# Optimization experiments

Measured on AMD Instinct MI355X. Metric: run time of the kernel, lower is better.

Reference implementation:

```python
import jax, jax.numpy as jnp
import numpy as np

T, D = 1024, 1024            # tokens, model dim
E, K = 16, 4                 # routed experts, top-k
G, TG = 4, 2                 # expert groups, limited (top) groups
INTER = 512                  # moe_inter_dim
SHARED_INTER = 2 * INTER     # n_shared_experts * moe_inter_dim
ROUTE_SCALE = 2.5
STD = 0.02


def setup_inputs() -> dict:
    key = jax.random.key(0)
    ks = jax.random.split(key, 9)
    return {
        "x": jax.random.normal(ks[0], (T, D), jnp.float32),
        "token_mask": jnp.ones((T,), jnp.bool_),
        "gate_w": jax.random.normal(ks[1], (E, D), jnp.float32) * STD,
        "gate_bias": jnp.zeros((E,), jnp.float32),  # e_score_correction_bias (zero-init)
        "gate_projs": jax.random.normal(ks[2], (E, INTER, D), jnp.float32) * STD,
        "up_projs": jax.random.normal(ks[3], (E, INTER, D), jnp.float32) * STD,
        "down_projs": jax.random.normal(ks[4], (E, D, INTER), jnp.float32) * STD,
        "shared_gate": jax.random.normal(ks[5], (SHARED_INTER, D), jnp.float32) * STD,
        "shared_up": jax.random.normal(ks[6], (SHARED_INTER, D), jnp.float32) * STD,
        "shared_down": jax.random.normal(ks[7], (D, SHARED_INTER), jnp.float32) * STD,
    }


def _route(x, gate_w, gate_bias):
    # sigmoid scoring with e_score_correction_bias + group-limited top-k (DeepSeek-V3 style)
    scores = jax.nn.sigmoid(x @ gate_w.T)                      # [T, E]
    s = (scores + gate_bias).reshape(T, G, E // G)             # bias-corrected, grouped
    group_scores = jax.lax.top_k(s, 2)[0].sum(-1)              # [T, G] sum of top-2 per group
    gidx = jax.lax.top_k(group_scores, TG)[1]                  # [T, TG]
    gmask = jax.nn.one_hot(gidx, G, dtype=s.dtype).sum(1)      # [T, G] selected-group mask
    masked = (s * gmask[:, :, None]).reshape(T, E)
    idx = jax.lax.top_k(masked, K)[1]                          # [T, K] expert indices
    w = jnp.take_along_axis(scores, idx, axis=1)               # gather original (unbiased) scores
    w = w / w.sum(-1, keepdims=True) * ROUTE_SCALE             # sigmoid renorm + route scale
    return w.astype(x.dtype), idx


def reference(x, token_mask, gate_w, gate_bias, gate_projs, up_projs,
              down_projs, shared_gate, shared_up, shared_down):
    w, idx = _route(x, gate_w, gate_bias)
    # dense combine weights [T, E]: combine[t, e] = sum_k w[t, k] * (idx[t, k] == e)
    combine = (jax.nn.one_hot(idx, E, dtype=x.dtype) * w[..., None]).sum(1)

    def body(acc, p):
        gp, up, dp, c = p                                      # per-expert SwiGLU
        inter = jax.nn.silu(x @ gp.T) * (x @ up.T)             # [T, INTER]
        return acc + c[:, None] * (inter @ dp.T), None

    routed, _ = jax.lax.scan(
        body, jnp.zeros_like(x), (gate_projs, up_projs, down_projs, combine.T))
    shared = (jax.nn.silu(x @ shared_gate.T) * (x @ shared_up.T)) @ shared_down.T
    return routed + shared
```

## Files before the change

kernel.cpp:

```cpp
#include <hip/hip_runtime.h>
#include <stdint.h>

#define TTOK 1024
#define DMODEL 1024
#define NEXP 16
#define TOPK 4
#define INTER 512
#define NSHI 1024
#define RSCALE 2.5f

typedef __bf16 bf16;
typedef __bf16 bf16x8 __attribute__((ext_vector_type(8)));
typedef __bf16 bf16x4 __attribute__((ext_vector_type(4)));
typedef float f32x4 __attribute__((ext_vector_type(4)));

#define APLANE 2064
#define BPLANE 1040

#define OFF_GP 0L
#define OFF_UP 8388608L
#define OFF_DP 16777216L
#define OFF_SG 25165824L
#define OFF_SU 26214400L
#define OFF_SD 27262976L
#define WTOT   28311552L

#define SCORES_BLOCKS 256
#define CONV_BLOCKS 27648

#define LGKM_BAR()                                            \
  do {                                                        \
    asm volatile("s_waitcnt lgkmcnt(0)" ::: "memory");        \
    __builtin_amdgcn_s_barrier();                             \
  } while (0)

__global__ __launch_bounds__(256)
void prep_kernel(const float* __restrict__ x, const float* __restrict__ gw,
                 float* __restrict__ scores, bf16* __restrict__ xbf,
                 const float* __restrict__ s0, const float* __restrict__ s1,
                 const float* __restrict__ s2, const float* __restrict__ s3,
                 const float* __restrict__ s4, const float* __restrict__ s5,
                 bf16* __restrict__ dst) {
  __shared__ float red[256];
  const int b = blockIdx.x;
  const int tid = threadIdx.x;
  if (b < SCORES_BLOCKS) {
    const long xb = (long)b * 1024;
#pragma unroll
    for (int p = 0; p < 4; ++p) {
      const long j = xb + p * 256 + tid;
      const float4 v = ((const float4*)x)[j];
      bf16x4 o;
      o.x = (bf16)v.x; o.y = (bf16)v.y; o.z = (bf16)v.z; o.w = (bf16)v.w;
      ((bf16x4*)xbf)[j] = o;
    }
    const int kq = tid >> 6;
    const int lane = tid & 63;
    const int tl = lane >> 4;
    const int e = lane & 15;
    const long token = (long)b * 4 + tl;
    float acc = 0.f;
    const int dbase = kq * 256;
#pragma unroll 8
    for (int i = 0; i < 256; i += 4) {
      const int d = dbase + i;
      const float4 xv = *(const float4*)&x[token * DMODEL + d];
      const float4 wv = *(const float4*)&gw[e * DMODEL + d];
      acc += xv.x * wv.x + xv.y * wv.y + xv.z * wv.z + xv.w * wv.w;
    }
    red[tid] = acc;
    __syncthreads();
    if (kq == 0) {
      const float s = red[lane] + red[64 + lane] + red[128 + lane] + red[192 + lane];
      scores[token * 16 + e] = s;
    }
  } else {
    const long i = (long)(b - SCORES_BLOCKS) * 256 + tid;
    const float* src;
    long local;
    if (i < 2097152)      { src = s0; local = i; }
    else if (i < 4194304) { src = s1; local = i - 2097152; }
    else if (i < 6291456) { src = s2; local = i - 4194304; }
    else if (i < 6553600) { src = s3; local = i - 6291456; }
    else if (i < 6815744) { src = s4; local = i - 6553600; }
    else                  { src = s5; local = i - 6815744; }
    const float4 v = ((const float4*)src)[local];
    bf16x4 o;
    o.x = (bf16)v.x; o.y = (bf16)v.y; o.z = (bf16)v.z; o.w = (bf16)v.w;
    ((bf16x4*)dst)[i] = o;
  }
}

__global__ __launch_bounds__(1024)
void route_kernel(const float* __restrict__ scores, const float* __restrict__ gb,
                  float* __restrict__ tokW, int* __restrict__ slotTok,
                  int* __restrict__ tokSlot, int* __restrict__ offs,
                  int* __restrict__ tileE, int* __restrict__ tileR,
                  int* __restrict__ tileCnt) {
  __shared__ int cnt[NEXP], cur[NEXP];
  const int t = threadIdx.x;
  if (t < NEXP) cnt[t] = 0;
  __syncthreads();
  float sc[NEXP], s[NEXP];
#pragma unroll
  for (int e = 0; e < NEXP; ++e) {
    const float l = scores[t * NEXP + e];
    sc[e] = 1.f / (1.f + expf(-l));
    s[e] = sc[e] + gb[e];
  }
  float gsc[4];
#pragma unroll
  for (int g = 0; g < 4; ++g) {
    const float a = s[4 * g], b = s[4 * g + 1], c = s[4 * g + 2], d = s[4 * g + 3];
    gsc[g] = fmaxf(fmaxf(fmaxf(a + b, a + c), fmaxf(a + d, b + c)),
                   fmaxf(b + d, c + d));
  }
  int g0 = 0;
  for (int g = 1; g < 4; ++g) if (gsc[g] > gsc[g0]) g0 = g;
  int g1 = (g0 == 0) ? 1 : 0;
  for (int g = 0; g < 4; ++g) if (g != g0 && gsc[g] > gsc[g1]) g1 = g;
  float m[NEXP];
#pragma unroll
  for (int e = 0; e < NEXP; ++e) {
    const int g = e >> 2;
    m[e] = (g == g0 || g == g1) ? s[e] : -1.f;
  }
  int idx[TOPK]; float wv[TOPK]; float wsum = 0.f;
  for (int k = 0; k < TOPK; ++k) {
    int am = 0; float best = m[0];
    for (int e2 = 1; e2 < NEXP; ++e2)
      if (m[e2] > best) { best = m[e2]; am = e2; }
    idx[k] = am; wv[k] = sc[am]; wsum += sc[am]; m[am] = -2.f;
  }
#pragma unroll
  for (int k = 0; k < TOPK; ++k) atomicAdd(&cnt[idx[k]], 1);
  __syncthreads();
  if (t == 0) {
    int acc = 0;
#pragma unroll
    for (int e = 0; e < NEXP; ++e) {
      offs[e] = acc; cur[e] = acc; acc += cnt[e];
    }
    offs[NEXP] = acc;
    int tc = 0;
    int roff = 0;
    for (int e = 0; e < NEXP; ++e) {
      const int end = roff + cnt[e];
      for (int r = roff; r < end; r += 128) { tileE[tc] = e; tileR[tc] = r; ++tc; }
      roff = end;
    }
    for (int r = 0; r < TTOK; r += 128) { tileE[tc] = NEXP; tileR[tc] = r; ++tc; }
    tileCnt[0] = tc;
  }
  __syncthreads();
  const float scl = RSCALE / wsum;
#pragma unroll
  for (int k = 0; k < TOPK; ++k) {
    const int slot = atomicAdd(&cur[idx[k]], 1);
    slotTok[slot] = t;
    tokSlot[t * TOPK + k] = slot;
    tokW[t * TOPK + k] = wv[k] * scl;
  }
}

__global__ __launch_bounds__(256, 2)
void gateup_gemm(const bf16* __restrict__ xbf, const int* __restrict__ slotTok,
                 const int* __restrict__ offs, const int* __restrict__ tileE,
                 const int* __restrict__ tileR, const int* __restrict__ tileCnt,
                 const bf16* __restrict__ wbf,
                 bf16* __restrict__ interR, bf16* __restrict__ interS) {
  const int y = blockIdx.y;
  if (y >= tileCnt[0]) return;
  const int e = tileE[y];
  const bool shd = (e == NEXP);
  const int n0 = blockIdx.x * 64;
  if (!shd && n0 >= INTER) return;
  const int rowStart = tileR[y];
  const int rowEnd = shd ? rowStart + 128 : offs[e + 1];
  const bf16* wgp = shd ? wbf + OFF_SG : wbf + OFF_GP + (long)e * INTER * DMODEL;
  const bf16* wup = shd ? wbf + OFF_SU : wbf + OFF_UP + (long)e * INTER * DMODEL;

  __shared__ __attribute__((aligned(16))) char As[8 * APLANE];
  __shared__ __attribute__((aligned(16))) char Bg[8 * BPLANE];
  __shared__ __attribute__((aligned(16))) char Bu[8 * BPLANE];
  __shared__ int tokS[128];

  const int tid = threadIdx.x;
  if (tid < 128) {
    const int r = rowStart + tid;
    tokS[tid] = shd ? r : slotTok[r < rowEnd ? r : rowStart];
  }
  __syncthreads();

  const int arw = tid >> 3;
  const int aoct = tid & 7;
  const bf16* aSrc[4];
#pragma unroll
  for (int p = 0; p < 4; ++p)
    aSrc[p] = xbf + (long)tokS[p * 32 + arw] * DMODEL + aoct * 8;

  const int bu_ = tid >> 7;
  const int u = tid & 127;
  const int brw = u >> 3;
  const int boct = u & 7;
  const bf16* bSrc = (bu_ ? wup : wgp) + (long)(n0 + brw) * DMODEL + boct * 8;
  char* bDst = bu_ ? Bu : Bg;

  const int lane = tid & 63;
  const int wv = tid >> 6;
  const int q = lane >> 4;
  const int l15 = lane & 15;
  const int wm = (wv >> 1) * 64;
  const int wn = (wv & 1) * 32;

  const f32x4 fz = {0.f, 0.f, 0.f, 0.f};
  f32x4 accG[4][2], accU[4][2];
#pragma unroll
  for (int i = 0; i < 4; ++i)
#pragma unroll
    for (int j = 0; j < 2; ++j) { accG[i][j] = fz; accU[i][j] = fz; }

  bf16x8 av[4];
  bf16x8 bv[4];
#pragma unroll
  for (int p = 0; p < 4; ++p) av[p] = *(const bf16x8*)(aSrc[p]);
#pragma unroll
  for (int p = 0; p < 4; ++p)
    bv[p] = *(const bf16x8*)(bSrc + (long)(p * 16) * DMODEL);

  for (int k0 = 0; k0 < DMODEL; k0 += 64) {
    LGKM_BAR();
#pragma unroll
    for (int p = 0; p < 4; ++p)
      *(bf16x8*)(As + aoct * APLANE + (p * 32 + arw) * 16) = av[p];
#pragma unroll
    for (int p = 0; p < 4; ++p)
      *(bf16x8*)(bDst + boct * BPLANE + (p * 16 + brw) * 16) = bv[p];
    const int kn = k0 + 64;
    if (kn < DMODEL) {
#pragma unroll
      for (int p = 0; p < 4; ++p) av[p] = *(const bf16x8*)(aSrc[p] + kn);
#pragma unroll
      for (int p = 0; p < 4; ++p)
        bv[p] = *(const bf16x8*)(bSrc + (long)(p * 16) * DMODEL + kn);
    }
    LGKM_BAR();
#pragma unroll
    for (int kb = 0; kb < 2; ++kb) {
      bf16x8 aF[4];
#pragma unroll
      for (int mi = 0; mi < 4; ++mi)
        aF[mi] = *(const bf16x8*)(As + (4 * kb + q) * APLANE + (wm + 16 * mi + l15) * 16);
#pragma unroll
      for (int ni = 0; ni < 2; ++ni) {
        const int br = wn + 16 * ni + l15;
        const bf16x8 gF = *(const bf16x8*)(Bg + (4 * kb + q) * BPLANE + br * 16);
        const bf16x8 uF = *(const bf16x8*)(Bu + (4 * kb + q) * BPLANE + br * 16);
#pragma unroll
        for (int mi = 0; mi < 4; ++mi) {
          accG[mi][ni] = __builtin_amdgcn_mfma_f32_16x16x32_bf16(aF[mi], gF, accG[mi][ni], 0, 0, 0);
          accU[mi][ni] = __builtin_amdgcn_mfma_f32_16x16x32_bf16(aF[mi], uF, accU[mi][ni], 0, 0, 0);
        }
      }
    }
  }

  bf16* outI = shd ? interS : interR;
  const int ldI = shd ? NSHI : INTER;
#pragma unroll
  for (int mi = 0; mi < 4; ++mi)
#pragma unroll
    for (int r = 0; r < 4; ++r) {
      const int rowLoc = wm + 16 * mi + q * 4 + r;
      const int row = rowStart + rowLoc;
      if (row < rowEnd) {
#pragma unroll
        for (int ni = 0; ni < 2; ++ni) {
          const float gg = accG[mi][ni][r];
          const float uu = accU[mi][ni][r];
          const float sv = gg / (1.f + __expf(-gg)) * uu;
          outI[(long)row * ldI + (n0 + wn + 16 * ni + l15)] = (bf16)sv;
        }
      }
    }
}

__global__ __launch_bounds__(256, 2)
void down_gemm(const bf16* __restrict__ interR, const bf16* __restrict__ interS,
               const int* __restrict__ offs, const int* __restrict__ tileE,
               const int* __restrict__ tileR, const int* __restrict__ tileCnt,
               const bf16* __restrict__ wbf,
               float* __restrict__ dsR, float* __restrict__ dsS) {
  const int y = blockIdx.y;
  if (y >= tileCnt[0]) return;
  const int e = tileE[y];
  const bool shd = (e == NEXP);
  const int n0 = blockIdx.x * 64;
  const int rowStart = tileR[y];
  const int rowEnd = shd ? rowStart + 128 : offs[e + 1];
  const int Kd = shd ? NSHI : INTER;
  const bf16* A = shd ? interS : interR;
  const bf16* wd = shd ? wbf + OFF_SD : wbf + OFF_DP + (long)e * DMODEL * INTER;

  __shared__ __attribute__((aligned(16))) char As[8 * APLANE];
  __shared__ __attribute__((aligned(16))) char Bs[8 * BPLANE];

  const int tid = threadIdx.x;
  const int arw = tid >> 3;
  const int aoct = tid & 7;
  const bf16* aSrc[4];
#pragma unroll
  for (int p = 0; p < 4; ++p)
    aSrc[p] = A + (long)(rowStart + p * 32 + arw) * Kd + aoct * 8;

  const int brw = tid >> 3;
  const int boct = tid & 7;
  const bf16* bSrc = wd + (long)(n0 + brw) * Kd + boct * 8;

  const int lane = tid & 63;
  const int wv = tid >> 6;
  const int q = lane >> 4;
  const int l15 = lane & 15;
  const int wm = (wv >> 1) * 64;
  const int wn = (wv & 1) * 32;

  const f32x4 fz = {0.f, 0.f, 0.f, 0.f};
  f32x4 acc[4][2];
#pragma unroll
  for (int i = 0; i < 4; ++i)
#pragma unroll
    for (int j = 0; j < 2; ++j) acc[i][j] = fz;

  bf16x8 av[4];
  bf16x8 bv[2];
#pragma unroll
  for (int p = 0; p < 4; ++p) av[p] = *(const bf16x8*)(aSrc[p]);
#pragma unroll
  for (int p = 0; p < 2; ++p)
    bv[p] = *(const bf16x8*)(bSrc + (long)(p * 32) * Kd);

  for (int k0 = 0; k0 < Kd; k0 += 64) {
    LGKM_BAR();
#pragma unroll
    for (int p = 0; p < 4; ++p)
      *(bf16x8*)(As + aoct * APLANE + (p * 32 + arw) * 16) = av[p];
#pragma unroll
    for (int p = 0; p < 2; ++p)
      *(bf16x8*)(Bs + boct * BPLANE + (p * 32 + brw) * 16) = bv[p];
    const int kn = k0 + 64;
    if (kn < Kd) {
#pragma unroll
      for (int p = 0; p < 4; ++p) av[p] = *(const bf16x8*)(aSrc[p] + kn);
#pragma unroll
      for (int p = 0; p < 2; ++p)
        bv[p] = *(const bf16x8*)(bSrc + (long)(p * 32) * Kd + kn);
    }
    LGKM_BAR();
#pragma unroll
    for (int kb = 0; kb < 2; ++kb) {
      bf16x8 aF[4];
#pragma unroll
      for (int mi = 0; mi < 4; ++mi)
        aF[mi] = *(const bf16x8*)(As + (4 * kb + q) * APLANE + (wm + 16 * mi + l15) * 16);
#pragma unroll
      for (int ni = 0; ni < 2; ++ni) {
        const bf16x8 bF = *(const bf16x8*)(Bs + (4 * kb + q) * BPLANE + (wn + 16 * ni + l15) * 16);
#pragma unroll
        for (int mi = 0; mi < 4; ++mi)
          acc[mi][ni] = __builtin_amdgcn_mfma_f32_16x16x32_bf16(aF[mi], bF, acc[mi][ni], 0, 0, 0);
      }
    }
  }

  float* dst = shd ? dsS : dsR;
#pragma unroll
  for (int mi = 0; mi < 4; ++mi)
#pragma unroll
    for (int r = 0; r < 4; ++r) {
      const int rowLoc = wm + 16 * mi + q * 4 + r;
      const int row = rowStart + rowLoc;
      if (row < rowEnd) {
#pragma unroll
        for (int ni = 0; ni < 2; ++ni)
          dst[(long)row * DMODEL + (n0 + wn + 16 * ni + l15)] = acc[mi][ni][r];
      }
    }
}

__global__ __launch_bounds__(256)
void combine_kernel(const float* __restrict__ dsR, const float* __restrict__ dsS,
                    const int* __restrict__ tokSlot, const float* __restrict__ tokW,
                    float* __restrict__ out) {
  const int t = blockIdx.x;
  const int j = threadIdx.x;
  float4 v = ((const float4*)(dsS + (long)t * DMODEL))[j];
#pragma unroll
  for (int k = 0; k < TOPK; ++k) {
    const int s = tokSlot[t * TOPK + k];
    const float w = tokW[t * TOPK + k];
    const float4 r = ((const float4*)(dsR + (long)s * DMODEL))[j];
    v.x += w * r.x; v.y += w * r.y; v.z += w * r.z; v.w += w * r.w;
  }
  ((float4*)(out + (long)t * DMODEL))[j] = v;
}

extern "C" void kernel_launch(void* const* d_in, const int* in_sizes, int n_in,
                              void* d_out, int out_size, void* d_ws, size_t ws_size,
                              hipStream_t stream) {
  const float* x  = (const float*)d_in[0];
  const float* gw = (const float*)d_in[2];
  const float* gb = (const float*)d_in[3];
  const float* gp = (const float*)d_in[4];
  const float* up = (const float*)d_in[5];
  const float* dp = (const float*)d_in[6];
  const float* sg = (const float*)d_in[7];
  const float* su = (const float*)d_in[8];
  const float* sd = (const float*)d_in[9];
  float* out = (float*)d_out;

  char* base = (char*)d_ws;
  size_t off = 0;
  auto alloc = [&](size_t bytes) -> char* {
    off = (off + 255) & ~(size_t)255;
    char* p = base + off;
    off += bytes;
    return p;
  };
  bf16* wbf = (bf16*)alloc((size_t)WTOT * 2);
  bf16* xbf = (bf16*)alloc((size_t)TTOK * DMODEL * 2);
  bf16* interR = (bf16*)alloc((size_t)(TTOK * TOPK + 128) * INTER * 2);
  bf16* interS = (bf16*)alloc((size_t)TTOK * NSHI * 2);
  float* dsR = (float*)alloc((size_t)TTOK * TOPK * DMODEL * 4);
  float* dsS = (float*)alloc((size_t)TTOK * DMODEL * 4);
  float* scores = (float*)alloc((size_t)TTOK * NEXP * 4);
  float* tokW = (float*)alloc(TTOK * TOPK * 4);
  int* slotTok = (int*)alloc(TTOK * TOPK * 4);
  int* tokSlot = (int*)alloc(TTOK * TOPK * 4);
  int* offs = (int*)alloc((NEXP + 1) * 4);
  int* tileE = (int*)alloc(72 * 4);
  int* tileR = (int*)alloc(72 * 4);
  int* tileCnt = (int*)alloc(4);

  prep_kernel<<<SCORES_BLOCKS + CONV_BLOCKS, 256, 0, stream>>>(
      x, gw, scores, xbf, gp, up, dp, sg, su, sd, wbf);
  route_kernel<<<1, 1024, 0, stream>>>(scores, gb, tokW, slotTok, tokSlot,
                                       offs, tileE, tileR, tileCnt);

  gateup_gemm<<<dim3(16, 56, 1), 256, 0, stream>>>(
      xbf, slotTok, offs, tileE, tileR, tileCnt, wbf, interR, interS);
  down_gemm<<<dim3(16, 56, 1), 256, 0, stream>>>(
      interR, interS, offs, tileE, tileR, tileCnt, wbf, dsR, dsS);
  combine_kernel<<<TTOK, 256, 0, stream>>>(dsR, dsS, tokSlot, tokW, out);
}
```

Before: 219.9 us.

## Convert routed expert weights in-GEMM and fuse combine via atomic scatter

```diff
diff --git a/kernel.cpp b/kernel.cpp
--- a/kernel.cpp
+++ b/kernel.cpp
@@ -17,16 +17,13 @@
 #define APLANE 2064
 #define BPLANE 1040
 
-#define OFF_GP 0L
-#define OFF_UP 8388608L
-#define OFF_DP 16777216L
-#define OFF_SG 25165824L
-#define OFF_SU 26214400L
-#define OFF_SD 27262976L
-#define WTOT   28311552L
+#define OFF_SG2 0L
+#define OFF_SU2 1048576L
+#define OFF_SD2 2097152L
+#define WTOT2   3145728L
 
 #define SCORES_BLOCKS 256
-#define CONV_BLOCKS 27648
+#define CONV_BLOCKS 3072
 
 #define LGKM_BAR()                                            \
   do {                                                        \
@@ -37,10 +34,8 @@
 __global__ __launch_bounds__(256)
 void prep_kernel(const float* __restrict__ x, const float* __restrict__ gw,
                  float* __restrict__ scores, bf16* __restrict__ xbf,
-                 const float* __restrict__ s0, const float* __restrict__ s1,
-                 const float* __restrict__ s2, const float* __restrict__ s3,
-                 const float* __restrict__ s4, const float* __restrict__ s5,
-                 bf16* __restrict__ dst) {
+                 const float* __restrict__ sg, const float* __restrict__ su,
+                 const float* __restrict__ sd, bf16* __restrict__ wbf) {
   __shared__ float red[256];
   const int b = blockIdx.x;
   const int tid = threadIdx.x;
@@ -78,25 +73,21 @@
     const long i = (long)(b - SCORES_BLOCKS) * 256 + tid;
     const float* src;
     long local;
-    if (i < 2097152)      { src = s0; local = i; }
-    else if (i < 4194304) { src = s1; local = i - 2097152; }
-    else if (i < 6291456) { src = s2; local = i - 4194304; }
-    else if (i < 6553600) { src = s3; local = i - 6291456; }
-    else if (i < 6815744) { src = s4; local = i - 6553600; }
-    else                  { src = s5; local = i - 6815744; }
+    if (i < 262144L)      { src = sg; local = i; }
+    else if (i < 524288L) { src = su; local = i - 262144L; }
+    else                  { src = sd; local = i - 524288L; }
     const float4 v = ((const float4*)src)[local];
     bf16x4 o;
     o.x = (bf16)v.x; o.y = (bf16)v.y; o.z = (bf16)v.z; o.w = (bf16)v.w;
-    ((bf16x4*)dst)[i] = o;
+    ((bf16x4*)wbf)[i] = o;
   }
 }
 
 __global__ __launch_bounds__(1024)
 void route_kernel(const float* __restrict__ scores, const float* __restrict__ gb,
-                  float* __restrict__ tokW, int* __restrict__ slotTok,
-                  int* __restrict__ tokSlot, int* __restrict__ offs,
-                  int* __restrict__ tileE, int* __restrict__ tileR,
-                  int* __restrict__ tileCnt) {
+                  float* __restrict__ slotW, int* __restrict__ slotTok,
+                  int* __restrict__ offs, int* __restrict__ tileE,
+                  int* __restrict__ tileR, int* __restrict__ tileCnt) {
   __shared__ int cnt[NEXP], cur[NEXP];
   const int t = threadIdx.x;
   if (t < NEXP) cnt[t] = 0;
@@ -158,8 +149,7 @@
   for (int k = 0; k < TOPK; ++k) {
     const int slot = atomicAdd(&cur[idx[k]], 1);
     slotTok[slot] = t;
-    tokSlot[t * TOPK + k] = slot;
-    tokW[t * TOPK + k] = wv[k] * scl;
+    slotW[slot] = wv[k] * scl;
   }
 }
 
@@ -167,6 +157,7 @@
 void gateup_gemm(const bf16* __restrict__ xbf, const int* __restrict__ slotTok,
                  const int* __restrict__ offs, const int* __restrict__ tileE,
                  const int* __restrict__ tileR, const int* __restrict__ tileCnt,
+                 const float* __restrict__ Wg, const float* __restrict__ Wu,
                  const bf16* __restrict__ wbf,
                  bf16* __restrict__ interR, bf16* __restrict__ interS) {
   const int y = blockIdx.y;
@@ -177,8 +168,6 @@
   if (!shd && n0 >= INTER) return;
   const int rowStart = tileR[y];
   const int rowEnd = shd ? rowStart + 128 : offs[e + 1];
-  const bf16* wgp = shd ? wbf + OFF_SG : wbf + OFF_GP + (long)e * INTER * DMODEL;
-  const bf16* wup = shd ? wbf + OFF_SU : wbf + OFF_UP + (long)e * INTER * DMODEL;
 
   __shared__ __attribute__((aligned(16))) char As[8 * APLANE];
   __shared__ __attribute__((aligned(16))) char Bg[8 * BPLANE];
@@ -201,9 +190,6 @@
 
   const int bu_ = tid >> 7;
   const int u = tid & 127;
-  const int brw = u >> 3;
-  const int boct = u & 7;
-  const bf16* bSrc = (bu_ ? wup : wgp) + (long)(n0 + brw) * DMODEL + boct * 8;
   char* bDst = bu_ ? Bu : Bg;
 
   const int lane = tid & 63;
@@ -220,46 +206,103 @@
 #pragma unroll
     for (int j = 0; j < 2; ++j) { accG[i][j] = fz; accU[i][j] = fz; }
 
-  bf16x8 av[4];
-  bf16x8 bv[4];
-#pragma unroll
-  for (int p = 0; p < 4; ++p) av[p] = *(const bf16x8*)(aSrc[p]);
-#pragma unroll
-  for (int p = 0; p < 4; ++p)
-    bv[p] = *(const bf16x8*)(bSrc + (long)(p * 16) * DMODEL);
-
-  for (int k0 = 0; k0 < DMODEL; k0 += 64) {
-    LGKM_BAR();
+  if (shd) {
+    const int brw = u >> 3;
+    const int boct = u & 7;
+    const bf16* bSrc = (bu_ ? wbf + OFF_SU2 : wbf + OFF_SG2)
+                       + (long)(n0 + brw) * DMODEL + boct * 8;
+    bf16x8 av[4], bv[4];
+#pragma unroll
+    for (int p = 0; p < 4; ++p) av[p] = *(const bf16x8*)(aSrc[p]);
 #pragma unroll
     for (int p = 0; p < 4; ++p)
-      *(bf16x8*)(As + aoct * APLANE + (p * 32 + arw) * 16) = av[p];
-#pragma unroll
-    for (int p = 0; p < 4; ++p)
-      *(bf16x8*)(bDst + boct * BPLANE + (p * 16 + brw) * 16) = bv[p];
-    const int kn = k0 + 64;
-    if (kn < DMODEL) {
-#pragma unroll
-      for (int p = 0; p < 4; ++p) av[p] = *(const bf16x8*)(aSrc[p] + kn);
+      bv[p] = *(const bf16x8*)(bSrc + (long)(p * 16) * DMODEL);
+    for (int k0 = 0; k0 < DMODEL; k0 += 64) {
+      LGKM_BAR();
 #pragma unroll
       for (int p = 0; p < 4; ++p)
-        bv[p] = *(const bf16x8*)(bSrc + (long)(p * 16) * DMODEL + kn);
-    }
-    LGKM_BAR();
-#pragma unroll
-    for (int kb = 0; kb < 2; ++kb) {
-      bf16x8 aF[4];
-#pragma unroll
-      for (int mi = 0; mi < 4; ++mi)
-        aF[mi] = *(const bf16x8*)(As + (4 * kb + q) * APLANE + (wm + 16 * mi + l15) * 16);
-#pragma unroll
-      for (int ni = 0; ni < 2; ++ni) {
-        const int br = wn + 16 * ni + l15;
-        const bf16x8 gF = *(const bf16x8*)(Bg + (4 * kb + q) * BPLANE + br * 16);
-        const bf16x8 uF = *(const bf16x8*)(Bu + (4 * kb + q) * BPLANE + br * 16);
-#pragma unroll
-        for (int mi = 0; mi < 4; ++mi) {
-          accG[mi][ni] = __builtin_amdgcn_mfma_f32_16x16x32_bf16(aF[mi], gF, accG[mi][ni], 0, 0, 0);
-          accU[mi][ni] = __builtin_amdgcn_mfma_f32_16x16x32_bf16(aF[mi], uF, accU[mi][ni], 0, 0, 0);
+        *(bf16x8*)(As + aoct * APLANE + (p * 32 + arw) * 16) = av[p];
+#pragma unroll
+      for (int p = 0; p < 4; ++p)
+        *(bf16x8*)(bDst + boct * BPLANE + (p * 16 + brw) * 16) = bv[p];
+      const int kn = k0 + 64;
+      if (kn < DMODEL) {
+#pragma unroll
+        for (int p = 0; p < 4; ++p) av[p] = *(const bf16x8*)(aSrc[p] + kn);
+#pragma unroll
+        for (int p = 0; p < 4; ++p)
+          bv[p] = *(const bf16x8*)(bSrc + (long)(p * 16) * DMODEL + kn);
+      }
+      LGKM_BAR();
+#pragma unroll
+      for (int kb = 0; kb < 2; ++kb) {
+        bf16x8 aF[4];
+#pragma unroll
+        for (int mi = 0; mi < 4; ++mi)
+          aF[mi] = *(const bf16x8*)(As + (4 * kb + q) * APLANE + (wm + 16 * mi + l15) * 16);
+#pragma unroll
+        for (int ni = 0; ni < 2; ++ni) {
+          const int br = wn + 16 * ni + l15;
+          const bf16x8 gF = *(const bf16x8*)(Bg + (4 * kb + q) * BPLANE + br * 16);
+          const bf16x8 uF = *(const bf16x8*)(Bu + (4 * kb + q) * BPLANE + br * 16);
+#pragma unroll
+          for (int mi = 0; mi < 4; ++mi) {
+            accG[mi][ni] = __builtin_amdgcn_mfma_f32_16x16x32_bf16(aF[mi], gF, accG[mi][ni], 0, 0, 0);
+            accU[mi][ni] = __builtin_amdgcn_mfma_f32_16x16x32_bf16(aF[mi], uF, accU[mi][ni], 0, 0, 0);
+          }
+        }
+      }
+    }
+  } else {
+    const int brw = u >> 4;
+    const int bf4 = u & 15;
+    const int boct = bf4 >> 1;
+    const int bhalf = bf4 & 1;
+    const float* bSrc = (bu_ ? Wu : Wg) + (long)e * INTER * DMODEL
+                        + (long)n0 * DMODEL + bf4 * 4;
+    bf16x8 av[4];
+    float4 bv[8];
+#pragma unroll
+    for (int p = 0; p < 4; ++p) av[p] = *(const bf16x8*)(aSrc[p]);
+#pragma unroll
+    for (int p = 0; p < 8; ++p)
+      bv[p] = *(const float4*)(bSrc + (long)(p * 8 + brw) * DMODEL);
+    for (int k0 = 0; k0 < DMODEL; k0 += 64) {
+      LGKM_BAR();
+#pragma unroll
+      for (int p = 0; p < 4; ++p)
+        *(bf16x8*)(As + aoct * APLANE + (p * 32 + arw) * 16) = av[p];
+#pragma unroll
+      for (int p = 0; p < 8; ++p) {
+        bf16x4 w;
+        w.x = (bf16)bv[p].x; w.y = (bf16)bv[p].y; w.z = (bf16)bv[p].z; w.w = (bf16)bv[p].w;
+        *(bf16x4*)(bDst + boct * BPLANE + (p * 8 + brw) * 16 + bhalf * 8) = w;
+      }
+      const int kn = k0 + 64;
+      if (kn < DMODEL) {
+#pragma unroll
+        for (int p = 0; p < 4; ++p) av[p] = *(const bf16x8*)(aSrc[p] + kn);
+#pragma unroll
+        for (int p = 0; p < 8; ++p)
+          bv[p] = *(const float4*)(bSrc + (long)(p * 8 + brw) * DMODEL + kn);
+      }
+      LGKM_BAR();
+#pragma unroll
+      for (int kb = 0; kb < 2; ++kb) {
+        bf16x8 aF[4];
+#pragma unroll
+        for (int mi = 0; mi < 4; ++mi)
+          aF[mi] = *(const bf16x8*)(As + (4 * kb + q) * APLANE + (wm + 16 * mi + l15) * 16);
+#pragma unroll
+        for (int ni = 0; ni < 2; ++ni) {
+          const int br = wn + 16 * ni + l15;
+          const bf16x8 gF = *(const bf16x8*)(Bg + (4 * kb + q) * BPLANE + br * 16);
+          const bf16x8 uF = *(const bf16x8*)(Bu + (4 * kb + q) * BPLANE + br * 16);
+#pragma unroll
+          for (int mi = 0; mi < 4; ++mi) {
+            accG[mi][ni] = __builtin_amdgcn_mfma_f32_16x16x32_bf16(aF[mi], gF, accG[mi][ni], 0, 0, 0);
+            accU[mi][ni] = __builtin_amdgcn_mfma_f32_16x16x32_bf16(aF[mi], uF, accU[mi][ni], 0, 0, 0);
+          }
         }
       }
     }
@@ -289,8 +332,9 @@
 void down_gemm(const bf16* __restrict__ interR, const bf16* __restrict__ interS,
                const int* __restrict__ offs, const int* __restrict__ tileE,
                const int* __restrict__ tileR, const int* __restrict__ tileCnt,
-               const bf16* __restrict__ wbf,
-               float* __restrict__ dsR, float* __restrict__ dsS) {
+               const float* __restrict__ Wd, const bf16* __restrict__ wbf,
+               const int* __restrict__ slotTok, const float* __restrict__ slotW,
+               float* __restrict__ out) {
   const int y = blockIdx.y;
   if (y >= tileCnt[0]) return;
   const int e = tileE[y];
@@ -300,7 +344,6 @@
   const int rowEnd = shd ? rowStart + 128 : offs[e + 1];
   const int Kd = shd ? NSHI : INTER;
   const bf16* A = shd ? interS : interR;
-  const bf16* wd = shd ? wbf + OFF_SD : wbf + OFF_DP + (long)e * DMODEL * INTER;
 
   __shared__ __attribute__((aligned(16))) char As[8 * APLANE];
   __shared__ __attribute__((aligned(16))) char Bs[8 * BPLANE];
@@ -312,10 +355,6 @@
 #pragma unroll
   for (int p = 0; p < 4; ++p)
     aSrc[p] = A + (long)(rowStart + p * 32 + arw) * Kd + aoct * 8;
-
-  const int brw = tid >> 3;
-  const int boct = tid & 7;
-  const bf16* bSrc = wd + (long)(n0 + brw) * Kd + boct * 8;
 
   const int lane = tid & 63;
   const int wv = tid >> 6;
@@ -331,48 +370,98 @@
 #pragma unroll
     for (int j = 0; j < 2; ++j) acc[i][j] = fz;
 
-  bf16x8 av[4];
-  bf16x8 bv[2];
-#pragma unroll
-  for (int p = 0; p < 4; ++p) av[p] = *(const bf16x8*)(aSrc[p]);
-#pragma unroll
-  for (int p = 0; p < 2; ++p)
-    bv[p] = *(const bf16x8*)(bSrc + (long)(p * 32) * Kd);
-
-  for (int k0 = 0; k0 < Kd; k0 += 64) {
-    LGKM_BAR();
+  if (shd) {
+    const int brw = tid >> 3;
+    const int boct = tid & 7;
+    const bf16* bSrc = wbf + OFF_SD2 + (long)(n0 + brw) * Kd + boct * 8;
+    bf16x8 av[4], bv[2];
+#pragma unroll
+    for (int p = 0; p < 4; ++p) av[p] = *(const bf16x8*)(aSrc[p]);
+#pragma unroll
+    for (int p = 0; p < 2; ++p)
+      bv[p] = *(const bf16x8*)(bSrc + (long)(p * 32) * Kd);
+    for (int k0 = 0; k0 < Kd; k0 += 64) {
+      LGKM_BAR();
+#pragma unroll
+      for (int p = 0; p < 4; ++p)
+        *(bf16x8*)(As + aoct * APLANE + (p * 32 + arw) * 16) = av[p];
+#pragma unroll
+      for (int p = 0; p < 2; ++p)
+        *(bf16x8*)(Bs + boct * BPLANE + (p * 32 + brw) * 16) = bv[p];
+      const int kn = k0 + 64;
+      if (kn < Kd) {
+#pragma unroll
+        for (int p = 0; p < 4; ++p) av[p] = *(const bf16x8*)(aSrc[p] + kn);
+#pragma unroll
+        for (int p = 0; p < 2; ++p)
+          bv[p] = *(const bf16x8*)(bSrc + (long)(p * 32) * Kd + kn);
+      }
+      LGKM_BAR();
+#pragma unroll
+      for (int kb = 0; kb < 2; ++kb) {
+        bf16x8 aF[4];
+#pragma unroll
+        for (int mi = 0; mi < 4; ++mi)
+          aF[mi] = *(const bf16x8*)(As + (4 * kb + q) * APLANE + (wm + 16 * mi + l15) * 16);
+#pragma unroll
+        for (int ni = 0; ni < 2; ++ni) {
+          const bf16x8 bF = *(const bf16x8*)(Bs + (4 * kb + q) * BPLANE + (wn + 16 * ni + l15) * 16);
+#pragma unroll
+          for (int mi = 0; mi < 4; ++mi)
+            acc[mi][ni] = __builtin_amdgcn_mfma_f32_16x16x32_bf16(aF[mi], bF, acc[mi][ni], 0, 0, 0);
+        }
+      }
+    }
+  } else {
+    const int brw = tid >> 4;
+    const int bf4 = tid & 15;
+    const int boct = bf4 >> 1;
+    const int bhalf = bf4 & 1;
+    const float* bSrc = Wd + (long)e * DMODEL * INTER + (long)n0 * Kd + bf4 * 4;
+    bf16x8 av[4];
+    float4 bv[4];
+#pragma unroll
+    for (int p = 0; p < 4; ++p) av[p] = *(const bf16x8*)(aSrc[p]);
 #pragma unroll
     for (int p = 0; p < 4; ++p)
-      *(bf16x8*)(As + aoct * APLANE + (p * 32 + arw) * 16) = av[p];
-#pragma unroll
-    for (int p = 0; p < 2; ++p)
-      *(bf16x8*)(Bs + boct * BPLANE + (p * 32 + brw) * 16) = bv[p];
-    const int kn = k0 + 64;
-    if (kn < Kd) {
-#pragma unroll
-      for (int p = 0; p < 4; ++p) av[p] = *(const bf16x8*)(aSrc[p] + kn);
-#pragma unroll
-      for (int p = 0; p < 2; ++p)
-        bv[p] = *(const bf16x8*)(bSrc + (long)(p * 32) * Kd + kn);
-    }
-    LGKM_BAR();
-#pragma unroll
-    for (int kb = 0; kb < 2; ++kb) {
-      bf16x8 aF[4];
-#pragma unroll
-      for (int mi = 0; mi < 4; ++mi)
-        aF[mi] = *(const bf16x8*)(As + (4 * kb + q) * APLANE + (wm + 16 * mi + l15) * 16);
-#pragma unroll
-      for (int ni = 0; ni < 2; ++ni) {
-        const bf16x8 bF = *(const bf16x8*)(Bs + (4 * kb + q) * BPLANE + (wn + 16 * ni + l15) * 16);
+      bv[p] = *(const float4*)(bSrc + (long)(p * 16 + brw) * Kd);
+    for (int k0 = 0; k0 < Kd; k0 += 64) {
+      LGKM_BAR();
+#pragma unroll
+      for (int p = 0; p < 4; ++p)
+        *(bf16x8*)(As + aoct * APLANE + (p * 32 + arw) * 16) = av[p];
+#pragma unroll
+      for (int p = 0; p < 4; ++p) {
+        bf16x4 w;
+        w.x = (bf16)bv[p].x; w.y = (bf16)bv[p].y; w.z = (bf16)bv[p].z; w.w = (bf16)bv[p].w;
+        *(bf16x4*)(Bs + boct * BPLANE + (p * 16 + brw) * 16 + bhalf * 8) = w;
+      }
+      const int kn = k0 + 64;
+      if (kn < Kd) {
+#pragma unroll
+        for (int p = 0; p < 4; ++p) av[p] = *(const bf16x8*)(aSrc[p] + kn);
+#pragma unroll
+        for (int p = 0; p < 4; ++p)
+          bv[p] = *(const float4*)(bSrc + (long)(p * 16 + brw) * Kd + kn);
+      }
+      LGKM_BAR();
+#pragma unroll
+      for (int kb = 0; kb < 2; ++kb) {
+        bf16x8 aF[4];
 #pragma unroll
         for (int mi = 0; mi < 4; ++mi)
-          acc[mi][ni] = __builtin_amdgcn_mfma_f32_16x16x32_bf16(aF[mi], bF, acc[mi][ni], 0, 0, 0);
-      }
-    }
-  }
-
-  float* dst = shd ? dsS : dsR;
+          aF[mi] = *(const bf16x8*)(As + (4 * kb + q) * APLANE + (wm + 16 * mi + l15) * 16);
+#pragma unroll
+        for (int ni = 0; ni < 2; ++ni) {
+          const bf16x8 bF = *(const bf16x8*)(Bs + (4 * kb + q) * BPLANE + (wn + 16 * ni + l15) * 16);
+#pragma unroll
+          for (int mi = 0; mi < 4; ++mi)
+            acc[mi][ni] = __builtin_amdgcn_mfma_f32_16x16x32_bf16(aF[mi], bF, acc[mi][ni], 0, 0, 0);
+        }
+      }
+    }
+  }
+
 #pragma unroll
   for (int mi = 0; mi < 4; ++mi)
 #pragma unroll
@@ -380,28 +469,21 @@
       const int rowLoc = wm + 16 * mi + q * 4 + r;
       const int row = rowStart + rowLoc;
       if (row < rowEnd) {
-#pragma unroll
-        for (int ni = 0; ni < 2; ++ni)
-          dst[(long)row * DMODEL + (n0 + wn + 16 * ni + l15)] = acc[mi][ni][r];
-      }
-    }
-}
-
-__global__ __launch_bounds__(256)
-void combine_kernel(const float* __restrict__ dsR, const float* __restrict__ dsS,
-                    const int* __restrict__ tokSlot, const float* __restrict__ tokW,
-                    float* __restrict__ out) {
-  const int t = blockIdx.x;
-  const int j = threadIdx.x;
-  float4 v = ((const float4*)(dsS + (long)t * DMODEL))[j];
-#pragma unroll
-  for (int k = 0; k < TOPK; ++k) {
-    const int s = tokSlot[t * TOPK + k];
-    const float w = tokW[t * TOPK + k];
-    const float4 r = ((const float4*)(dsR + (long)s * DMODEL))[j];
-    v.x += w * r.x; v.y += w * r.y; v.z += w * r.z; v.w += w * r.w;
-  }
-  ((float4*)(out + (long)t * DMODEL))[j] = v;
+        if (shd) {
+#pragma unroll
+          for (int ni = 0; ni < 2; ++ni)
+            atomicAdd(&out[(long)row * DMODEL + (n0 + wn + 16 * ni + l15)],
+                      acc[mi][ni][r]);
+        } else {
+          const int tok = slotTok[row];
+          const float w = slotW[row];
+#pragma unroll
+          for (int ni = 0; ni < 2; ++ni)
+            atomicAdd(&out[(long)tok * DMODEL + (n0 + wn + 16 * ni + l15)],
+                      w * acc[mi][ni][r]);
+        }
+      }
+    }
 }
 
 extern "C" void kernel_launch(void* const* d_in, const int* in_sizes, int n_in,
@@ -426,29 +508,27 @@
     off += bytes;
     return p;
   };
-  bf16* wbf = (bf16*)alloc((size_t)WTOT * 2);
+  bf16* wbf = (bf16*)alloc((size_t)WTOT2 * 2);
   bf16* xbf = (bf16*)alloc((size_t)TTOK * DMODEL * 2);
   bf16* interR = (bf16*)alloc((size_t)(TTOK * TOPK + 128) * INTER * 2);
   bf16* interS = (bf16*)alloc((size_t)TTOK * NSHI * 2);
-  float* dsR = (float*)alloc((size_t)TTOK * TOPK * DMODEL * 4);
-  float* dsS = (float*)alloc((size_t)TTOK * DMODEL * 4);
   float* scores = (float*)alloc((size_t)TTOK * NEXP * 4);
-  float* tokW = (float*)alloc(TTOK * TOPK * 4);
+  float* slotW = (float*)alloc(TTOK * TOPK * 4);
   int* slotTok = (int*)alloc(TTOK * TOPK * 4);
-  int* tokSlot = (int*)alloc(TTOK * TOPK * 4);
   int* offs = (int*)alloc((NEXP + 1) * 4);
   int* tileE = (int*)alloc(72 * 4);
   int* tileR = (int*)alloc(72 * 4);
   int* tileCnt = (int*)alloc(4);
 
+  hipMemsetAsync(out, 0, (size_t)TTOK * DMODEL * 4, stream);
+
   prep_kernel<<<SCORES_BLOCKS + CONV_BLOCKS, 256, 0, stream>>>(
-      x, gw, scores, xbf, gp, up, dp, sg, su, sd, wbf);
-  route_kernel<<<1, 1024, 0, stream>>>(scores, gb, tokW, slotTok, tokSlot,
+      x, gw, scores, xbf, sg, su, sd, wbf);
+  route_kernel<<<1, 1024, 0, stream>>>(scores, gb, slotW, slotTok,
                                        offs, tileE, tileR, tileCnt);
 
   gateup_gemm<<<dim3(16, 56, 1), 256, 0, stream>>>(
-      xbf, slotTok, offs, tileE, tileR, tileCnt, wbf, interR, interS);
+      xbf, slotTok, offs, tileE, tileR, tileCnt, gp, up, wbf, interR, interS);
   down_gemm<<<dim3(16, 56, 1), 256, 0, stream>>>(
-      interR, interS, offs, tileE, tileR, tileCnt, wbf, dsR, dsS);
-  combine_kernel<<<TTOK, 256, 0, stream>>>(dsR, dsS, tokSlot, tokW, out);
+      interR, interS, offs, tileE, tileR, tileCnt, dp, wbf, slotTok, slotW, out);
 }
```

Result: slower. 238.7 us (+8.5%).

## Load MFMA fragments directly from global memory, dropping LDS staging and barriers

Applied to the files above, without the earlier changes.

```diff
diff --git a/kernel.cpp b/kernel.cpp
--- a/kernel.cpp
+++ b/kernel.cpp
@@ -14,9 +14,6 @@
 typedef __bf16 bf16x4 __attribute__((ext_vector_type(4)));
 typedef float f32x4 __attribute__((ext_vector_type(4)));
 
-#define APLANE 2064
-#define BPLANE 1040
-
 #define OFF_GP 0L
 #define OFF_UP 8388608L
 #define OFF_DP 16777216L
@@ -27,12 +24,6 @@
 
 #define SCORES_BLOCKS 256
 #define CONV_BLOCKS 27648
-
-#define LGKM_BAR()                                            \
-  do {                                                        \
-    asm volatile("s_waitcnt lgkmcnt(0)" ::: "memory");        \
-    __builtin_amdgcn_s_barrier();                             \
-  } while (0)
 
 __global__ __launch_bounds__(256)
 void prep_kernel(const float* __restrict__ x, const float* __restrict__ gw,
@@ -180,32 +171,7 @@
   const bf16* wgp = shd ? wbf + OFF_SG : wbf + OFF_GP + (long)e * INTER * DMODEL;
   const bf16* wup = shd ? wbf + OFF_SU : wbf + OFF_UP + (long)e * INTER * DMODEL;
 
-  __shared__ __attribute__((aligned(16))) char As[8 * APLANE];
-  __shared__ __attribute__((aligned(16))) char Bg[8 * BPLANE];
-  __shared__ __attribute__((aligned(16))) char Bu[8 * BPLANE];
-  __shared__ int tokS[128];
-
   const int tid = threadIdx.x;
-  if (tid < 128) {
-    const int r = rowStart + tid;
-    tokS[tid] = shd ? r : slotTok[r < rowEnd ? r : rowStart];
-  }
-  __syncthreads();
-
-  const int arw = tid >> 3;
-  const int aoct = tid & 7;
-  const bf16* aSrc[4];
-#pragma unroll
-  for (int p = 0; p < 4; ++p)
-    aSrc[p] = xbf + (long)tokS[p * 32 + arw] * DMODEL + aoct * 8;
-
-  const int bu_ = tid >> 7;
-  const int u = tid & 127;
-  const int brw = u >> 3;
-  const int boct = u & 7;
-  const bf16* bSrc = (bu_ ? wup : wgp) + (long)(n0 + brw) * DMODEL + boct * 8;
-  char* bDst = bu_ ? Bu : Bg;
-
   const int lane = tid & 63;
   const int wv = tid >> 6;
   const int q = lane >> 4;
@@ -213,6 +179,21 @@
   const int wm = (wv >> 1) * 64;
   const int wn = (wv & 1) * 32;
 
+  const bf16* aP[4];
+#pragma unroll
+  for (int mi = 0; mi < 4; ++mi) {
+    const int r = rowStart + wm + 16 * mi + l15;
+    const int tok = shd ? r : slotTok[r < rowEnd ? r : rowStart];
+    aP[mi] = xbf + (long)tok * DMODEL + q * 8;
+  }
+  const bf16* gP[2]; const bf16* uP[2];
+#pragma unroll
+  for (int ni = 0; ni < 2; ++ni) {
+    const long nrow = n0 + wn + 16 * ni + l15;
+    gP[ni] = wgp + nrow * DMODEL + q * 8;
+    uP[ni] = wup + nrow * DMODEL + q * 8;
+  }
+
   const f32x4 fz = {0.f, 0.f, 0.f, 0.f};
   f32x4 accG[4][2], accU[4][2];
 #pragma unroll
@@ -220,47 +201,73 @@
 #pragma unroll
     for (int j = 0; j < 2; ++j) { accG[i][j] = fz; accU[i][j] = fz; }
 
-  bf16x8 av[4];
-  bf16x8 bv[4];
-#pragma unroll
-  for (int p = 0; p < 4; ++p) av[p] = *(const bf16x8*)(aSrc[p]);
-#pragma unroll
-  for (int p = 0; p < 4; ++p)
-    bv[p] = *(const bf16x8*)(bSrc + (long)(p * 16) * DMODEL);
-
-  for (int k0 = 0; k0 < DMODEL; k0 += 64) {
-    LGKM_BAR();
-#pragma unroll
-    for (int p = 0; p < 4; ++p)
-      *(bf16x8*)(As + aoct * APLANE + (p * 32 + arw) * 16) = av[p];
-#pragma unroll
-    for (int p = 0; p < 4; ++p)
-      *(bf16x8*)(bDst + boct * BPLANE + (p * 16 + brw) * 16) = bv[p];
-    const int kn = k0 + 64;
-    if (kn < DMODEL) {
-#pragma unroll
-      for (int p = 0; p < 4; ++p) av[p] = *(const bf16x8*)(aSrc[p] + kn);
-#pragma unroll
-      for (int p = 0; p < 4; ++p)
-        bv[p] = *(const bf16x8*)(bSrc + (long)(p * 16) * DMODEL + kn);
-    }
-    LGKM_BAR();
-#pragma unroll
-    for (int kb = 0; kb < 2; ++kb) {
-      bf16x8 aF[4];
-#pragma unroll
-      for (int mi = 0; mi < 4; ++mi)
-        aF[mi] = *(const bf16x8*)(As + (4 * kb + q) * APLANE + (wm + 16 * mi + l15) * 16);
-#pragma unroll
-      for (int ni = 0; ni < 2; ++ni) {
-        const int br = wn + 16 * ni + l15;
-        const bf16x8 gF = *(const bf16x8*)(Bg + (4 * kb + q) * BPLANE + br * 16);
-        const bf16x8 uF = *(const bf16x8*)(Bu + (4 * kb + q) * BPLANE + br * 16);
+  bf16x8 aFA[4], gFA[2], uFA[2], aFB[4], gFB[2], uFB[2];
+#pragma unroll
+  for (int mi = 0; mi < 4; ++mi) aFA[mi] = *(const bf16x8*)(aP[mi]);
+#pragma unroll
+  for (int ni = 0; ni < 2; ++ni) {
+    gFA[ni] = *(const bf16x8*)(gP[ni]);
+    uFA[ni] = *(const bf16x8*)(uP[ni]);
+  }
+#pragma unroll
+  for (int mi = 0; mi < 4; ++mi) aFB[mi] = *(const bf16x8*)(aP[mi] + 32);
+#pragma unroll
+  for (int ni = 0; ni < 2; ++ni) {
+    gFB[ni] = *(const bf16x8*)(gP[ni] + 32);
+    uFB[ni] = *(const bf16x8*)(uP[ni] + 32);
+  }
+
+  for (int k = 0; k < DMODEL; k += 64) {
+    {
+      const int kp = k + 64;
+      bf16x8 aT[4], gT[2], uT[2];
+      if (kp < DMODEL) {
+#pragma unroll
+        for (int mi = 0; mi < 4; ++mi) aT[mi] = *(const bf16x8*)(aP[mi] + kp);
+#pragma unroll
+        for (int ni = 0; ni < 2; ++ni) {
+          gT[ni] = *(const bf16x8*)(gP[ni] + kp);
+          uT[ni] = *(const bf16x8*)(uP[ni] + kp);
+        }
+      }
+#pragma unroll
+      for (int ni = 0; ni < 2; ++ni)
 #pragma unroll
         for (int mi = 0; mi < 4; ++mi) {
-          accG[mi][ni] = __builtin_amdgcn_mfma_f32_16x16x32_bf16(aF[mi], gF, accG[mi][ni], 0, 0, 0);
-          accU[mi][ni] = __builtin_amdgcn_mfma_f32_16x16x32_bf16(aF[mi], uF, accU[mi][ni], 0, 0, 0);
+          accG[mi][ni] = __builtin_amdgcn_mfma_f32_16x16x32_bf16(aFA[mi], gFA[ni], accG[mi][ni], 0, 0, 0);
+          accU[mi][ni] = __builtin_amdgcn_mfma_f32_16x16x32_bf16(aFA[mi], uFA[ni], accU[mi][ni], 0, 0, 0);
         }
+      if (kp < DMODEL) {
+#pragma unroll
+        for (int mi = 0; mi < 4; ++mi) aFA[mi] = aT[mi];
+#pragma unroll
+        for (int ni = 0; ni < 2; ++ni) { gFA[ni] = gT[ni]; uFA[ni] = uT[ni]; }
+      }
+    }
+    {
+      const int kp = k + 96;
+      bf16x8 aT[4], gT[2], uT[2];
+      if (kp < DMODEL) {
+#pragma unroll
+        for (int mi = 0; mi < 4; ++mi) aT[mi] = *(const bf16x8*)(aP[mi] + kp);
+#pragma unroll
+        for (int ni = 0; ni < 2; ++ni) {
+          gT[ni] = *(const bf16x8*)(gP[ni] + kp);
+          uT[ni] = *(const bf16x8*)(uP[ni] + kp);
+        }
+      }
+#pragma unroll
+      for (int ni = 0; ni < 2; ++ni)
+#pragma unroll
+        for (int mi = 0; mi < 4; ++mi) {
+          accG[mi][ni] = __builtin_amdgcn_mfma_f32_16x16x32_bf16(aFB[mi], gFB[ni], accG[mi][ni], 0, 0, 0);
+          accU[mi][ni] = __builtin_amdgcn_mfma_f32_16x16x32_bf16(aFB[mi], uFB[ni], accU[mi][ni], 0, 0, 0);
+        }
+      if (kp < DMODEL) {
+#pragma unroll
+        for (int mi = 0; mi < 4; ++mi) aFB[mi] = aT[mi];
+#pragma unroll
+        for (int ni = 0; ni < 2; ++ni) { gFB[ni] = gT[ni]; uFB[ni] = uT[ni]; }
       }
     }
   }
@@ -302,21 +309,7 @@
   const bf16* A = shd ? interS : interR;
   const bf16* wd = shd ? wbf + OFF_SD : wbf + OFF_DP + (long)e * DMODEL * INTER;
 
-  __shared__ __attribute__((aligned(16))) char As[8 * APLANE];
-  __shared__ __attribute__((aligned(16))) char Bs[8 * BPLANE];
-
   const int tid = threadIdx.x;
-  const int arw = tid >> 3;
-  const int aoct = tid & 7;
-  const bf16* aSrc[4];
-#pragma unroll
-  for (int p = 0; p < 4; ++p)
-    aSrc[p] = A + (long)(rowStart + p * 32 + arw) * Kd + aoct * 8;
-
-  const int brw = tid >> 3;
-  const int boct = tid & 7;
-  const bf16* bSrc = wd + (long)(n0 + brw) * Kd + boct * 8;
-
   const int lane = tid & 63;
   const int wv = tid >> 6;
   const int q = lane >> 4;
@@ -324,6 +317,15 @@
   const int wm = (wv >> 1) * 64;
   const int wn = (wv & 1) * 32;
 
+  const bf16* aP[4];
+#pragma unroll
+  for (int mi = 0; mi < 4; ++mi)
+    aP[mi] = A + (long)(rowStart + wm + 16 * mi + l15) * Kd + q * 8;
+  const bf16* bP[2];
+#pragma unroll
+  for (int ni = 0; ni < 2; ++ni)
+    bP[ni] = wd + (long)(n0 + wn + 16 * ni + l15) * Kd + q * 8;
+
   const f32x4 fz = {0.f, 0.f, 0.f, 0.f};
   f32x4 acc[4][2];
 #pragma unroll
@@ -331,43 +333,57 @@
 #pragma unroll
     for (int j = 0; j < 2; ++j) acc[i][j] = fz;
 
-  bf16x8 av[4];
-  bf16x8 bv[2];
-#pragma unroll
-  for (int p = 0; p < 4; ++p) av[p] = *(const bf16x8*)(aSrc[p]);
-#pragma unroll
-  for (int p = 0; p < 2; ++p)
-    bv[p] = *(const bf16x8*)(bSrc + (long)(p * 32) * Kd);
-
-  for (int k0 = 0; k0 < Kd; k0 += 64) {
-    LGKM_BAR();
-#pragma unroll
-    for (int p = 0; p < 4; ++p)
-      *(bf16x8*)(As + aoct * APLANE + (p * 32 + arw) * 16) = av[p];
-#pragma unroll
-    for (int p = 0; p < 2; ++p)
-      *(bf16x8*)(Bs + boct * BPLANE + (p * 32 + brw) * 16) = bv[p];
-    const int kn = k0 + 64;
-    if (kn < Kd) {
-#pragma unroll
-      for (int p = 0; p < 4; ++p) av[p] = *(const bf16x8*)(aSrc[p] + kn);
-#pragma unroll
-      for (int p = 0; p < 2; ++p)
-        bv[p] = *(const bf16x8*)(bSrc + (long)(p * 32) * Kd + kn);
-    }
-    LGKM_BAR();
-#pragma unroll
-    for (int kb = 0; kb < 2; ++kb) {
-      bf16x8 aF[4];
-#pragma unroll
-      for (int mi = 0; mi < 4; ++mi)
-        aF[mi] = *(const bf16x8*)(As + (4 * kb + q) * APLANE + (wm + 16 * mi + l15) * 16);
-#pragma unroll
-      for (int ni = 0; ni < 2; ++ni) {
-        const bf16x8 bF = *(const bf16x8*)(Bs + (4 * kb + q) * BPLANE + (wn + 16 * ni + l15) * 16);
+  bf16x8 aFA[4], bFA[2], aFB[4], bFB[2];
+#pragma unroll
+  for (int mi = 0; mi < 4; ++mi) aFA[mi] = *(const bf16x8*)(aP[mi]);
+#pragma unroll
+  for (int ni = 0; ni < 2; ++ni) bFA[ni] = *(const bf16x8*)(bP[ni]);
+#pragma unroll
+  for (int mi = 0; mi < 4; ++mi) aFB[mi] = *(const bf16x8*)(aP[mi] + 32);
+#pragma unroll
+  for (int ni = 0; ni < 2; ++ni) bFB[ni] = *(const bf16x8*)(bP[ni] + 32);
+
+  for (int k = 0; k < Kd; k += 64) {
+    {
+      const int kp = k + 64;
+      bf16x8 aT[4], bT[2];
+      if (kp < Kd) {
+#pragma unroll
+        for (int mi = 0; mi < 4; ++mi) aT[mi] = *(const bf16x8*)(aP[mi] + kp);
+#pragma unroll
+        for (int ni = 0; ni < 2; ++ni) bT[ni] = *(const bf16x8*)(bP[ni] + kp);
+      }
+#pragma unroll
+      for (int ni = 0; ni < 2; ++ni)
 #pragma unroll
         for (int mi = 0; mi < 4; ++mi)
-          acc[mi][ni] = __builtin_amdgcn_mfma_f32_16x16x32_bf16(aF[mi], bF, acc[mi][ni], 0, 0, 0);
+          acc[mi][ni] = __builtin_amdgcn_mfma_f32_16x16x32_bf16(aFA[mi], bFA[ni], acc[mi][ni], 0, 0, 0);
+      if (kp < Kd) {
+#pragma unroll
+        for (int mi = 0; mi < 4; ++mi) aFA[mi] = aT[mi];
+#pragma unroll
+        for (int ni = 0; ni < 2; ++ni) bFA[ni] = bT[ni];
+      }
+    }
+    {
+      const int kp = k + 96;
+      bf16x8 aT[4], bT[2];
+      if (kp < Kd) {
+#pragma unroll
+        for (int mi = 0; mi < 4; ++mi) aT[mi] = *(const bf16x8*)(aP[mi] + kp);
+#pragma unroll
+        for (int ni = 0; ni < 2; ++ni) bT[ni] = *(const bf16x8*)(bP[ni] + kp);
+      }
+#pragma unroll
+      for (int ni = 0; ni < 2; ++ni)
+#pragma unroll
+        for (int mi = 0; mi < 4; ++mi)
+          acc[mi][ni] = __builtin_amdgcn_mfma_f32_16x16x32_bf16(aFB[mi], bFB[ni], acc[mi][ni], 0, 0, 0);
+      if (kp < Kd) {
+#pragma unroll
+        for (int mi = 0; mi < 4; ++mi) aFB[mi] = aT[mi];
+#pragma unroll
+        for (int ni = 0; ni < 2; ++ni) bFB[ni] = bT[ni];
       }
     }
   }
```

Measured after the change: 304.5 us. +38.5%, slower.
